# Optimization experiments

Hardware: AMD Instinct MI355X
Metric: run time of the kernel (lower is better)

The kernel has to match this reference:

```python
import jax, jax.numpy as jnp
import numpy as np

N = 50000
E = 800000
NODE_C = 96
EDGE_C = 192
C1, C2, CMU = 125, 144, 163  # round(96+96*0.3), round(96+96*0.5), round(96+96*0.7)
DIVIDER = 10.0


def setup_inputs() -> dict:
    key = jax.random.key(0)
    ks = jax.random.split(key, 32)
    def w(k, i, o):
        return jax.random.normal(k, (i, o), jnp.float32) * (1.0 / np.sqrt(i))
    inp = {
        "x": jax.random.normal(ks[0], (N, NODE_C), jnp.float32),
        "edge_index": jax.random.randint(ks[1], (2, E), 0, N, dtype=jnp.int64),
        "eps_edge": jax.random.normal(ks[2], (N, CMU), jnp.float32),
        "eps_node": jax.random.normal(ks[3], (N, NODE_C), jnp.float32),
        "w1e": w(ks[4], NODE_C, C1), "b1e": jnp.zeros((C1,), jnp.float32),
        "w2e": w(ks[5], C1, C2),     "b2e": jnp.zeros((C2,), jnp.float32),
        "wme": w(ks[6], C2, CMU),    "bme": jnp.zeros((CMU,), jnp.float32),
        "wle": w(ks[7], C2, CMU),    "ble": jnp.zeros((CMU,), jnp.float32),
        "w4e": w(ks[8], CMU, EDGE_C),"b4e": jnp.zeros((EDGE_C,), jnp.float32),
        "w1n": w(ks[9], NODE_C, NODE_C), "b1n": jnp.zeros((NODE_C,), jnp.float32),
        "wmn": w(ks[10], NODE_C, NODE_C),"bmn": jnp.zeros((NODE_C,), jnp.float32),
        "wln": w(ks[11], NODE_C, NODE_C),"bln": jnp.zeros((NODE_C,), jnp.float32),
        "w5n": w(ks[12], NODE_C, NODE_C),"b5n": jnp.zeros((NODE_C,), jnp.float32),
    }
    return inp


def reference(x, edge_index, eps_edge, eps_node,
              w1e, b1e, w2e, b2e, wme, bme, wle, ble, w4e, b4e,
              w1n, b1n, wmn, bmn, wln, bln, w5n, b5n):
    row, col = edge_index[0], edge_index[1]
    n = x.shape[0]
    # GCN symmetric normalization with self-loops (deg counts incoming edges + 1)
    deg = jax.ops.segment_sum(jnp.ones(row.shape[0], x.dtype), col, num_segments=n) + 1.0
    dinv = deg ** -0.5
    coef = dinv[row] * dinv[col]          # [E]
    self_coef = (dinv * dinv)[:, None]    # [N,1] self-loop contribution

    def conv(h, W, b):
        hw = h @ W                                            # [N, out]
        agg = jax.ops.segment_sum(hw[row] * coef[:, None], col, num_segments=n)
        return agg + hw * self_coef + b

    # edge branch
    e = jax.nn.relu(conv(x, w1e, b1e))
    e = jax.nn.relu(conv(e, w2e, b2e))
    mu_e = conv(e, wme, bme)
    ls_e = conv(e, wle, ble)
    e = mu_e + eps_edge * jnp.exp(ls_e) / DIVIDER   # training-mode reparametrize
    edges = jax.nn.sigmoid(conv(e, w4e, b4e))

    # node branch
    nn_ = jax.nn.relu(conv(x, w1n, b1n))
    mu_n = conv(nn_, wmn, bmn)
    ls_n = conv(nn_, wln, bln)
    nn_ = mu_n + eps_node * jnp.exp(ls_n) / DIVIDER
    nodes = jax.nn.relu(conv(nn_, w5n, b5n))

    return edges, nodes
```

## Files before the change

### kernel.cpp

```cpp
#include <hip/hip_runtime.h>

typedef unsigned short u16;
typedef unsigned int u32;
typedef __bf16 bf16x8 __attribute__((ext_vector_type(8)));
typedef float f32x4 __attribute__((ext_vector_type(4)));

__device__ __forceinline__ u16 f2bf(float f) {
    u32 u = __float_as_uint(f);
    u32 r = (u + 0x7fffu + ((u >> 16) & 1u)) >> 16;
    return (u16)r;
}
__device__ __forceinline__ float bf2f(u16 v) { return __uint_as_float(((u32)v) << 16); }
__device__ __forceinline__ float bf_lo(u32 v) { return __uint_as_float(v << 16); }
__device__ __forceinline__ float bf_hi(u32 v) { return __uint_as_float(v & 0xffff0000u); }
__device__ __forceinline__ u32 pack2(float lo, float hi) {
    return (u32)f2bf(lo) | (((u32)f2bf(hi)) << 16);
}


__global__ void deg_kernel(const int* __restrict__ ei, int E, int* __restrict__ cnt) {
    int i = blockIdx.x * blockDim.x + threadIdx.x;
    if (i < E) atomicAdd(&cnt[ei[E + i]], 1);
}

__global__ void dinv_kernel(const int* __restrict__ cnt, float* __restrict__ dinv, int N) {
    int i = blockIdx.x * blockDim.x + threadIdx.x;
    if (i < N) dinv[i] = 1.0f / sqrtf((float)cnt[i] + 1.0f);
}

__global__ __launch_bounds__(256) void scan1_k(const int* __restrict__ cnt,
                                               int* __restrict__ offs,
                                               int* __restrict__ bsum, int N) {
    __shared__ int lds[256];
    int t = threadIdx.x;
    int idx0 = blockIdx.x * 1024 + t * 4;
    int v[4], s = 0;
#pragma unroll
    for (int k = 0; k < 4; k++) {
        int i = idx0 + k;
        v[k] = (i < N) ? cnt[i] : 0;
        s += v[k];
    }
    lds[t] = s;
    __syncthreads();
    for (int off = 1; off < 256; off <<= 1) {
        int u = 0;
        if (t >= off) u = lds[t - off];
        __syncthreads();
        lds[t] += u;
        __syncthreads();
    }
    int run = lds[t] - s;
#pragma unroll
    for (int k = 0; k < 4; k++) {
        int i = idx0 + k;
        if (i < N) offs[i] = run;
        run += v[k];
    }
    if (t == 255) bsum[blockIdx.x] = lds[255];
}

__global__ __launch_bounds__(256) void scan2_k(int* __restrict__ bsum, int* __restrict__ boff,
                                               int nb, int* __restrict__ totp) {
    __shared__ int lds[256];
    int t = threadIdx.x;
    int s = (t < nb) ? bsum[t] : 0;
    lds[t] = s;
    __syncthreads();
    for (int off = 1; off < 256; off <<= 1) {
        int u = 0;
        if (t >= off) u = lds[t - off];
        __syncthreads();
        lds[t] += u;
        __syncthreads();
    }
    if (t < nb) boff[t] = lds[t] - s;
    if (t == 255) *totp = lds[255];
}

__global__ void scan3_k(int* __restrict__ offs, int* __restrict__ cursor,
                        const int* __restrict__ boff, int N) {
    int i = blockIdx.x * blockDim.x + threadIdx.x;
    if (i < N) {
        int v = offs[i] + boff[i >> 10];
        offs[i] = v;
        cursor[i] = v;
    }
}

__global__ void fill_kernel(const int* __restrict__ ei, int E,
                            const float* __restrict__ dinv, int* __restrict__ cursor,
                            int* __restrict__ csr_src, float* __restrict__ csr_w) {
    int i = blockIdx.x * blockDim.x + threadIdx.x;
    if (i < E) {
        int r = ei[i];
        int c = ei[E + i];
        int pos = atomicAdd(&cursor[c], 1);
        csr_src[pos] = r;
        csr_w[pos] = dinv[r];
    }
}


__global__ void cvt_f2bf_k(const float* __restrict__ src, u16* __restrict__ dst, int npairs) {
    u32* d = (u32*)dst;
    for (int i = blockIdx.x * blockDim.x + threadIdx.x; i < npairs;
         i += blockDim.x * gridDim.x) {
        float lo = src[2 * i], hi = src[2 * i + 1];
        d[i] = pack2(lo, hi);
    }
}


struct PackArgs {
    const float* W[9];
    const float* B[9];
    int Kin[9], Nout[9], KS[9], NT[9], wOff[9], bOff[9];
};

__global__ void pack_weights(PackArgs pa, u16* __restrict__ wpack, float* __restrict__ bpack) {
    int L = blockIdx.y;
    int KS = pa.KS[L], NT = pa.NT[L], Kin = pa.Kin[L], Nout = pa.Nout[L];
    int wtot = KS * NT * 512;
    int btot = NT * 16;
    const float* W = pa.W[L];
    const float* Bb = pa.B[L];
    u16* wp = wpack + pa.wOff[L];
    float* bp = bpack + pa.bOff[L];
    for (int idx = blockIdx.x * blockDim.x + threadIdx.x; idx < wtot + btot;
         idx += blockDim.x * gridDim.x) {
        if (idx < wtot) {
            int j = idx & 7;
            int lane = (idx >> 3) & 63;
            int pos = idx >> 9;
            int jt = pos % NT;
            int ks = pos / NT;
            int k = ks * 32 + ((lane >> 4) & 3) * 8 + j;
            int n = jt * 16 + (lane & 15);
            u16 v = 0;
            if (k < Kin && n < Nout) v = f2bf(W[k * Nout + n]);
            wp[idx] = v;
        } else {
            int n = idx - wtot;
            float v = 0.f;
            if (n < Nout) v = Bb[n];
            bp[n] = v;
        }
    }
}


template <int C2>
__global__ __launch_bounds__(256) void propagate_k(const u16* __restrict__ h,
                                                   u16* __restrict__ out,
                                                   const float* __restrict__ dinv,
                                                   const int* __restrict__ offs,
                                                   const int* __restrict__ csr_src,
                                                   const float* __restrict__ csr_w, int N) {
    constexpr int Cp = C2 * 2;
    const int lane = threadIdx.x & 63;
    int wid = (blockIdx.x * blockDim.x + threadIdx.x) >> 6;
    int nw = (gridDim.x * blockDim.x) >> 6;
    constexpr bool HAS1 = (C2 > 64);
    const bool a0 = lane < (C2 < 64 ? C2 : 64);
    const bool a1 = HAS1 && (lane < C2 - 64);
    const int c0 = lane, c1 = lane + 64;
    for (int n = wid; n < N; n += nw) {
        float dn = dinv[n];
        int beg = offs[n], end = offs[n + 1];
        float x0 = 0.f, y0 = 0.f, x1 = 0.f, y1 = 0.f;
        {
            const u32* hp = (const u32*)(h + (size_t)n * Cp);
            if (a0) { u32 v = hp[c0]; x0 = dn * bf_lo(v); y0 = dn * bf_hi(v); }
            if (a1) { u32 v = hp[c1]; x1 = dn * bf_lo(v); y1 = dn * bf_hi(v); }
        }
        int e = beg;
        for (; e + 1 < end; e += 2) {
            int s0 = csr_src[e], s1 = csr_src[e + 1];
            float w0 = csr_w[e], w1 = csr_w[e + 1];
            const u32* p0 = (const u32*)(h + (size_t)s0 * Cp);
            const u32* p1 = (const u32*)(h + (size_t)s1 * Cp);
            if (a0) {
                u32 u = p0[c0], v = p1[c0];
                x0 = fmaf(w0, bf_lo(u), x0); y0 = fmaf(w0, bf_hi(u), y0);
                x0 = fmaf(w1, bf_lo(v), x0); y0 = fmaf(w1, bf_hi(v), y0);
            }
            if (a1) {
                u32 u = p0[c1], v = p1[c1];
                x1 = fmaf(w0, bf_lo(u), x1); y1 = fmaf(w0, bf_hi(u), y1);
                x1 = fmaf(w1, bf_lo(v), x1); y1 = fmaf(w1, bf_hi(v), y1);
            }
        }
        if (e < end) {
            int s0 = csr_src[e];
            float w0 = csr_w[e];
            const u32* p0 = (const u32*)(h + (size_t)s0 * Cp);
            if (a0) { u32 u = p0[c0]; x0 = fmaf(w0, bf_lo(u), x0); y0 = fmaf(w0, bf_hi(u), y0); }
            if (a1) { u32 u = p0[c1]; x1 = fmaf(w0, bf_lo(u), x1); y1 = fmaf(w0, bf_hi(u), y1); }
        }
        u32* op = (u32*)(out + (size_t)n * Cp);
        if (a0) op[c0] = pack2(dn * x0, dn * y0);
        if (a1) op[c1] = pack2(dn * x1, dn * y1);
    }
}


template <int KS, int NT, int OP, int OUTF>
__global__ __launch_bounds__(256) void gemm_k(const u16* __restrict__ A,
                                              const u16* __restrict__ Bp,
                                              const float* __restrict__ bias,
                                              void* __restrict__ Cv, int M, int ldc) {
    constexpr int Kp = KS * 32;
    const int lane = threadIdx.x & 63;
    const int wave = threadIdx.x >> 6;
    int m0 = (blockIdx.x * 4 + wave) * 16;
    if (m0 >= M) return;
    int row = m0 + (lane & 15);
    if (row >= M) row = M - 1;
    const u16* aptr = A + (size_t)row * Kp + ((lane >> 4) * 8);
    const u16* bptr = Bp + lane * 8;
    f32x4 acc[NT];
#pragma unroll
    for (int j = 0; j < NT; j++) acc[j] = (f32x4){0.f, 0.f, 0.f, 0.f};
#pragma unroll
    for (int ks = 0; ks < KS; ks++) {
        bf16x8 af = *(const bf16x8*)(aptr + ks * 32);
#pragma unroll
        for (int j = 0; j < NT; j++) {
            bf16x8 bf = *(const bf16x8*)(bptr + (ks * NT + j) * 512);
            acc[j] = __builtin_amdgcn_mfma_f32_16x16x32_bf16(af, bf, acc[j], 0, 0, 0);
        }
    }
    int mrow = m0 + (lane >> 4) * 4;
#pragma unroll
    for (int j = 0; j < NT; j++) {
        int n = j * 16 + (lane & 15);
        float b = bias[n];
#pragma unroll
        for (int r = 0; r < 4; r++) {
            int m = mrow + r;
            if (m < M) {
                float v = acc[j][r] + b;
                if (OP == 1) v = fmaxf(v, 0.f);
                if (OP == 2) v = 1.f / (1.f + expf(-v));
                if (OUTF) ((float*)Cv)[(size_t)m * ldc + n] = v;
                else ((u16*)Cv)[(size_t)m * ldc + n] = f2bf(v);
            }
        }
    }
}


template <int KS, int NT1, int NT2>
__global__ __launch_bounds__(256) void gemm_dual_relu_k(const u16* __restrict__ A,
                                                        const u16* __restrict__ Bp1,
                                                        const float* __restrict__ bias1,
                                                        u16* __restrict__ C1o, int ld1,
                                                        const u16* __restrict__ Bp2,
                                                        const float* __restrict__ bias2,
                                                        u16* __restrict__ C2o, int ld2, int M) {
    constexpr int Kp = KS * 32;
    const int lane = threadIdx.x & 63;
    const int wave = threadIdx.x >> 6;
    int m0 = (blockIdx.x * 4 + wave) * 16;
    if (m0 >= M) return;
    int row = m0 + (lane & 15);
    if (row >= M) row = M - 1;
    const u16* aptr = A + (size_t)row * Kp + ((lane >> 4) * 8);
    f32x4 acc1[NT1], acc2[NT2];
#pragma unroll
    for (int j = 0; j < NT1; j++) acc1[j] = (f32x4){0.f, 0.f, 0.f, 0.f};
#pragma unroll
    for (int j = 0; j < NT2; j++) acc2[j] = (f32x4){0.f, 0.f, 0.f, 0.f};
#pragma unroll
    for (int ks = 0; ks < KS; ks++) {
        bf16x8 af = *(const bf16x8*)(aptr + ks * 32);
#pragma unroll
        for (int j = 0; j < NT1; j++) {
            bf16x8 bf = *(const bf16x8*)(Bp1 + lane * 8 + (ks * NT1 + j) * 512);
            acc1[j] = __builtin_amdgcn_mfma_f32_16x16x32_bf16(af, bf, acc1[j], 0, 0, 0);
        }
#pragma unroll
        for (int j = 0; j < NT2; j++) {
            bf16x8 bf = *(const bf16x8*)(Bp2 + lane * 8 + (ks * NT2 + j) * 512);
            acc2[j] = __builtin_amdgcn_mfma_f32_16x16x32_bf16(af, bf, acc2[j], 0, 0, 0);
        }
    }
    int mrow = m0 + (lane >> 4) * 4;
#pragma unroll
    for (int j = 0; j < NT1; j++) {
        int n = j * 16 + (lane & 15);
        float b = bias1[n];
#pragma unroll
        for (int r = 0; r < 4; r++) {
            int m = mrow + r;
            if (m < M) C1o[(size_t)m * ld1 + n] = f2bf(fmaxf(acc1[j][r] + b, 0.f));
        }
    }
#pragma unroll
    for (int j = 0; j < NT2; j++) {
        int n = j * 16 + (lane & 15);
        float b = bias2[n];
#pragma unroll
        for (int r = 0; r < 4; r++) {
            int m = mrow + r;
            if (m < M) C2o[(size_t)m * ld2 + n] = f2bf(fmaxf(acc2[j][r] + b, 0.f));
        }
    }
}


template <int KS, int NT, int CLIM>
__global__ __launch_bounds__(256) void gemm_reparam_k(const u16* __restrict__ A,
                                                      const u16* __restrict__ BpM,
                                                      const float* __restrict__ biasM,
                                                      const u16* __restrict__ BpL,
                                                      const float* __restrict__ biasL,
                                                      const float* __restrict__ eps, int epsLd,
                                                      u16* __restrict__ out, int ldc, int M) {
    constexpr int Kp = KS * 32;
    const int lane = threadIdx.x & 63;
    const int wave = threadIdx.x >> 6;
    int m0 = (blockIdx.x * 4 + wave) * 16;
    if (m0 >= M) return;
    int row = m0 + (lane & 15);
    if (row >= M) row = M - 1;
    const u16* aptr = A + (size_t)row * Kp + ((lane >> 4) * 8);
    f32x4 accM[NT], accL[NT];
#pragma unroll
    for (int j = 0; j < NT; j++) {
        accM[j] = (f32x4){0.f, 0.f, 0.f, 0.f};
        accL[j] = (f32x4){0.f, 0.f, 0.f, 0.f};
    }
#pragma unroll
    for (int ks = 0; ks < KS; ks++) {
        bf16x8 af = *(const bf16x8*)(aptr + ks * 32);
#pragma unroll
        for (int j = 0; j < NT; j++) {
            bf16x8 bm = *(const bf16x8*)(BpM + lane * 8 + (ks * NT + j) * 512);
            accM[j] = __builtin_amdgcn_mfma_f32_16x16x32_bf16(af, bm, accM[j], 0, 0, 0);
            bf16x8 bl = *(const bf16x8*)(BpL + lane * 8 + (ks * NT + j) * 512);
            accL[j] = __builtin_amdgcn_mfma_f32_16x16x32_bf16(af, bl, accL[j], 0, 0, 0);
        }
    }
    int mrow = m0 + (lane >> 4) * 4;
#pragma unroll
    for (int j = 0; j < NT; j++) {
        int n = j * 16 + (lane & 15);
        float bm = biasM[n];
        float bl = biasL[n];
#pragma unroll
        for (int r = 0; r < 4; r++) {
            int m = mrow + r;
            if (m < M) {
                float v = 0.f;
                if (n < CLIM) {
                    float e = eps[(size_t)m * epsLd + n];
                    v = (accM[j][r] + bm) + e * expf(accL[j][r] + bl) * 0.1f;
                }
                out[(size_t)m * ldc + n] = f2bf(v);
            }
        }
    }
}


extern "C" void kernel_launch(void* const* d_in, const int* in_sizes, int n_in,
                              void* d_out, int out_size, void* d_ws, size_t ws_size,
                              hipStream_t stream) {
    const float* x = (const float*)d_in[0];
    const int* ei = (const int*)d_in[1];
    const float* eps_e = (const float*)d_in[2];
    const float* eps_n = (const float*)d_in[3];
    int N = in_sizes[0] / 96;
    int E = in_sizes[1] / 2;

    char* p = (char*)d_ws;
    auto alloc = [&](size_t bytes) -> char* {
        char* r = p;
        p += (bytes + 255) & ~(size_t)255;
        return r;
    };
    int* cnt = (int*)alloc((size_t)N * 4);
    float* dinv = (float*)alloc((size_t)N * 4);
    int* offs = (int*)alloc((size_t)(N + 1) * 4);
    int* cursor = (int*)alloc((size_t)N * 4);
    int* bsum = (int*)alloc(256 * 4);
    int* boff = (int*)alloc(256 * 4);
    int* csr_src = (int*)alloc((size_t)E * 4);
    float* csr_w = (float*)alloc((size_t)E * 4);
    u16* wpack = (u16*)alloc(167936 * 2);
    float* bpack = (float*)alloc(1248 * 4);
    size_t bufBytes = (size_t)N * 192 * 2;
    u16* bufA = (u16*)alloc(bufBytes);
    u16* bufB = (u16*)alloc(bufBytes);
    u16* bufC = (u16*)alloc(bufBytes);
    u16* bufD = (u16*)alloc(bufBytes);

    hipMemsetAsync(cnt, 0, (size_t)N * 4, stream);
    int gE = (E + 255) / 256, gN = (N + 255) / 256;
    deg_kernel<<<gE, 256, 0, stream>>>(ei, E, cnt);
    dinv_kernel<<<gN, 256, 0, stream>>>(cnt, dinv, N);
    int nb = (N + 1023) / 1024;
    scan1_k<<<nb, 256, 0, stream>>>(cnt, offs, bsum, N);
    scan2_k<<<1, 256, 0, stream>>>(bsum, boff, nb, offs + N);
    scan3_k<<<gN, 256, 0, stream>>>(offs, cursor, boff, N);
    fill_kernel<<<gE, 256, 0, stream>>>(ei, E, dinv, cursor, csr_src, csr_w);

    static const int wi[9] = {4, 6, 8, 10, 12, 14, 16, 18, 20};
    static const int bi[9] = {5, 7, 9, 11, 13, 15, 17, 19, 21};
    static const int Kin[9] = {96, 125, 144, 144, 163, 96, 96, 96, 96};
    static const int Nout[9] = {125, 144, 163, 163, 192, 96, 96, 96, 96};
    static const int KSa[9] = {3, 4, 5, 5, 6, 3, 3, 3, 3};
    static const int NTa[9] = {8, 10, 12, 12, 12, 6, 6, 6, 6};
    static const int wOff[9] = {0, 12288, 32768, 63488, 94208, 131072, 140288, 149504, 158720};
    static const int bOff[9] = {0, 128, 288, 480, 672, 864, 960, 1056, 1152};
    PackArgs pa;
    for (int i = 0; i < 9; i++) {
        pa.W[i] = (const float*)d_in[wi[i]];
        pa.B[i] = (const float*)d_in[bi[i]];
        pa.Kin[i] = Kin[i]; pa.Nout[i] = Nout[i];
        pa.KS[i] = KSa[i];  pa.NT[i] = NTa[i];
        pa.wOff[i] = wOff[i]; pa.bOff[i] = bOff[i];
    }
    pack_weights<<<dim3(32, 9), 256, 0, stream>>>(pa, wpack, bpack);

    const int gp = 2048;
    const int gg = (N + 63) / 64;

    cvt_f2bf_k<<<2048, 256, 0, stream>>>(x, bufD, N * 48);
    propagate_k<48><<<gp, 256, 0, stream>>>(bufD, bufA, dinv, offs, csr_src, csr_w, N);
    gemm_dual_relu_k<3, 8, 6><<<gg, 256, 0, stream>>>(bufA, wpack + 0, bpack + 0, bufC, 128,
                                                      wpack + 131072, bpack + 864, bufB, 96, N);
    propagate_k<64><<<gp, 256, 0, stream>>>(bufC, bufA, dinv, offs, csr_src, csr_w, N);
    gemm_k<4, 10, 1, 0><<<gg, 256, 0, stream>>>(bufA, wpack + 12288, bpack + 128, bufC, N, 160);
    propagate_k<80><<<gp, 256, 0, stream>>>(bufC, bufA, dinv, offs, csr_src, csr_w, N);
    gemm_reparam_k<5, 12, 163><<<gg, 256, 0, stream>>>(bufA, wpack + 32768, bpack + 288,
                                                       wpack + 63488, bpack + 480,
                                                       eps_e, 163, bufC, 192, N);
    propagate_k<96><<<gp, 256, 0, stream>>>(bufC, bufD, dinv, offs, csr_src, csr_w, N);
    gemm_k<6, 12, 2, 1><<<gg, 256, 0, stream>>>(bufD, wpack + 94208, bpack + 672, (float*)d_out, N, 192);
    propagate_k<48><<<gp, 256, 0, stream>>>(bufB, bufA, dinv, offs, csr_src, csr_w, N);
    gemm_reparam_k<3, 6, 96><<<gg, 256, 0, stream>>>(bufA, wpack + 140288, bpack + 960,
                                                     wpack + 149504, bpack + 1056,
                                                     eps_n, 96, bufC, 96, N);
    propagate_k<48><<<gp, 256, 0, stream>>>(bufC, bufA, dinv, offs, csr_src, csr_w, N);
    gemm_k<3, 6, 1, 1><<<gg, 256, 0, stream>>>(bufA, wpack + 158720, bpack + 1152,
                                               (float*)d_out + (size_t)N * 192, N, 96);
}
```

Baseline: 792.6 us.

## Split GEMM output columns across blockIdx.y and prefetch bf16 eps before MFMA loop

Each GEMM kernel now launches a 2D grid, with blockIdx.y choosing half of the output column tiles. This doubles the number of blocks and halves the accumulators per wave, which should improve occupancy and latency hiding. The dual-relu kernel sends its two weight sets to separate y-blocks. The eps noise tensors are converted to bf16 up front, and the reparam kernels load them into registers before the matmul so the load overlaps with compute. The cost is extra conversion launches, A rows read twice, and bf16 rounding of eps.

```diff
diff --git a/kernel.cpp b/kernel.cpp
--- a/kernel.cpp
+++ b/kernel.cpp
@@ -27,6 +27,7 @@
     int i = blockIdx.x * blockDim.x + threadIdx.x;
     if (i < N) dinv[i] = 1.0f / sqrtf((float)cnt[i] + 1.0f);
 }
+
 
 __global__ __launch_bounds__(256) void scan1_k(const int* __restrict__ cnt,
                                                int* __restrict__ offs,
@@ -205,36 +206,43 @@
 }
 
 
-template <int KS, int NT, int OP, int OUTF>
+template <int KS, int NTtot, int NTH>
+__device__ __forceinline__ void gemm_body(const u16* A, const u16* Bp, int jBase,
+                                          f32x4* acc, int m0, int M, int lane) {
+    constexpr int Kp = KS * 32;
+    int row = m0 + (lane & 15);
+    if (row >= M) row = M - 1;
+    const u16* aptr = A + (size_t)row * Kp + ((lane >> 4) * 8);
+    const u16* bptr = Bp + lane * 8;
+#pragma unroll
+    for (int j = 0; j < NTH; j++) acc[j] = (f32x4){0.f, 0.f, 0.f, 0.f};
+#pragma unroll
+    for (int ks = 0; ks < KS; ks++) {
+        bf16x8 af = *(const bf16x8*)(aptr + ks * 32);
+#pragma unroll
+        for (int j = 0; j < NTH; j++) {
+            bf16x8 bf = *(const bf16x8*)(bptr + (ks * NTtot + jBase + j) * 512);
+            acc[j] = __builtin_amdgcn_mfma_f32_16x16x32_bf16(af, bf, acc[j], 0, 0, 0);
+        }
+    }
+}
+
+template <int KS, int NTtot, int NTH, int OP, int OUTF>
 __global__ __launch_bounds__(256) void gemm_k(const u16* __restrict__ A,
                                               const u16* __restrict__ Bp,
                                               const float* __restrict__ bias,
                                               void* __restrict__ Cv, int M, int ldc) {
-    constexpr int Kp = KS * 32;
     const int lane = threadIdx.x & 63;
     const int wave = threadIdx.x >> 6;
+    const int jBase = blockIdx.y * NTH;
     int m0 = (blockIdx.x * 4 + wave) * 16;
     if (m0 >= M) return;
-    int row = m0 + (lane & 15);
-    if (row >= M) row = M - 1;
-    const u16* aptr = A + (size_t)row * Kp + ((lane >> 4) * 8);
-    const u16* bptr = Bp + lane * 8;
-    f32x4 acc[NT];
-#pragma unroll
-    for (int j = 0; j < NT; j++) acc[j] = (f32x4){0.f, 0.f, 0.f, 0.f};
-#pragma unroll
-    for (int ks = 0; ks < KS; ks++) {
-        bf16x8 af = *(const bf16x8*)(aptr + ks * 32);
-#pragma unroll
-        for (int j = 0; j < NT; j++) {
-            bf16x8 bf = *(const bf16x8*)(bptr + (ks * NT + j) * 512);
-            acc[j] = __builtin_amdgcn_mfma_f32_16x16x32_bf16(af, bf, acc[j], 0, 0, 0);
-        }
-    }
+    f32x4 acc[NTH];
+    gemm_body<KS, NTtot, NTH>(A, Bp, jBase, acc, m0, M, lane);
     int mrow = m0 + (lane >> 4) * 4;
 #pragma unroll
-    for (int j = 0; j < NT; j++) {
-        int n = j * 16 + (lane & 15);
+    for (int j = 0; j < NTH; j++) {
+        int n = (jBase + j) * 16 + (lane & 15);
         float b = bias[n];
 #pragma unroll
         for (int r = 0; r < 4; r++) {
@@ -250,7 +258,6 @@
     }
 }
 
-
 template <int KS, int NT1, int NT2>
 __global__ __launch_bounds__(256) void gemm_dual_relu_k(const u16* __restrict__ A,
                                                         const u16* __restrict__ Bp1,
@@ -259,76 +266,72 @@
                                                         const u16* __restrict__ Bp2,
                                                         const float* __restrict__ bias2,
                                                         u16* __restrict__ C2o, int ld2, int M) {
-    constexpr int Kp = KS * 32;
     const int lane = threadIdx.x & 63;
     const int wave = threadIdx.x >> 6;
     int m0 = (blockIdx.x * 4 + wave) * 16;
     if (m0 >= M) return;
-    int row = m0 + (lane & 15);
-    if (row >= M) row = M - 1;
-    const u16* aptr = A + (size_t)row * Kp + ((lane >> 4) * 8);
-    f32x4 acc1[NT1], acc2[NT2];
-#pragma unroll
-    for (int j = 0; j < NT1; j++) acc1[j] = (f32x4){0.f, 0.f, 0.f, 0.f};
-#pragma unroll
-    for (int j = 0; j < NT2; j++) acc2[j] = (f32x4){0.f, 0.f, 0.f, 0.f};
-#pragma unroll
-    for (int ks = 0; ks < KS; ks++) {
-        bf16x8 af = *(const bf16x8*)(aptr + ks * 32);
+    int mrow = m0 + (lane >> 4) * 4;
+    if (blockIdx.y == 0) {
+        f32x4 acc[NT1];
+        gemm_body<KS, NT1, NT1>(A, Bp1, 0, acc, m0, M, lane);
 #pragma unroll
         for (int j = 0; j < NT1; j++) {
-            bf16x8 bf = *(const bf16x8*)(Bp1 + lane * 8 + (ks * NT1 + j) * 512);
-            acc1[j] = __builtin_amdgcn_mfma_f32_16x16x32_bf16(af, bf, acc1[j], 0, 0, 0);
-        }
+            int n = j * 16 + (lane & 15);
+            float b = bias1[n];
+#pragma unroll
+            for (int r = 0; r < 4; r++) {
+                int m = mrow + r;
+                if (m < M) C1o[(size_t)m * ld1 + n] = f2bf(fmaxf(acc[j][r] + b, 0.f));
+            }
+        }
+    } else {
+        f32x4 acc[NT2];
+        gemm_body<KS, NT2, NT2>(A, Bp2, 0, acc, m0, M, lane);
 #pragma unroll
         for (int j = 0; j < NT2; j++) {
-            bf16x8 bf = *(const bf16x8*)(Bp2 + lane * 8 + (ks * NT2 + j) * 512);
-            acc2[j] = __builtin_amdgcn_mfma_f32_16x16x32_bf16(af, bf, acc2[j], 0, 0, 0);
-        }
-    }
-    int mrow = m0 + (lane >> 4) * 4;
-#pragma unroll
-    for (int j = 0; j < NT1; j++) {
-        int n = j * 16 + (lane & 15);
-        float b = bias1[n];
-#pragma unroll
-        for (int r = 0; r < 4; r++) {
-            int m = mrow + r;
-            if (m < M) C1o[(size_t)m * ld1 + n] = f2bf(fmaxf(acc1[j][r] + b, 0.f));
-        }
-    }
-#pragma unroll
-    for (int j = 0; j < NT2; j++) {
-        int n = j * 16 + (lane & 15);
-        float b = bias2[n];
-#pragma unroll
-        for (int r = 0; r < 4; r++) {
-            int m = mrow + r;
-            if (m < M) C2o[(size_t)m * ld2 + n] = f2bf(fmaxf(acc2[j][r] + b, 0.f));
-        }
-    }
-}
-
-
-template <int KS, int NT, int CLIM>
+            int n = j * 16 + (lane & 15);
+            float b = bias2[n];
+#pragma unroll
+            for (int r = 0; r < 4; r++) {
+                int m = mrow + r;
+                if (m < M) C2o[(size_t)m * ld2 + n] = f2bf(fmaxf(acc[j][r] + b, 0.f));
+            }
+        }
+    }
+}
+
+template <int KS, int NTtot, int NTH, int CLIM>
 __global__ __launch_bounds__(256) void gemm_reparam_k(const u16* __restrict__ A,
                                                       const u16* __restrict__ BpM,
                                                       const float* __restrict__ biasM,
                                                       const u16* __restrict__ BpL,
                                                       const float* __restrict__ biasL,
-                                                      const float* __restrict__ eps, int epsLd,
+                                                      const u16* __restrict__ epsb,
                                                       u16* __restrict__ out, int ldc, int M) {
-    constexpr int Kp = KS * 32;
     const int lane = threadIdx.x & 63;
     const int wave = threadIdx.x >> 6;
+    const int jBase = blockIdx.y * NTH;
     int m0 = (blockIdx.x * 4 + wave) * 16;
     if (m0 >= M) return;
+    int mrow = m0 + (lane >> 4) * 4;
+    float epsv[NTH * 4];
+#pragma unroll
+    for (int j = 0; j < NTH; j++) {
+        int n = (jBase + j) * 16 + (lane & 15);
+#pragma unroll
+        for (int r = 0; r < 4; r++) {
+            int m = mrow + r;
+            if (m >= M) m = M - 1;
+            epsv[j * 4 + r] = (n < CLIM) ? bf2f(epsb[(size_t)m * CLIM + n]) : 0.f;
+        }
+    }
+    constexpr int Kp = KS * 32;
     int row = m0 + (lane & 15);
     if (row >= M) row = M - 1;
     const u16* aptr = A + (size_t)row * Kp + ((lane >> 4) * 8);
-    f32x4 accM[NT], accL[NT];
-#pragma unroll
-    for (int j = 0; j < NT; j++) {
+    f32x4 accM[NTH], accL[NTH];
+#pragma unroll
+    for (int j = 0; j < NTH; j++) {
         accM[j] = (f32x4){0.f, 0.f, 0.f, 0.f};
         accL[j] = (f32x4){0.f, 0.f, 0.f, 0.f};
     }
@@ -336,17 +339,16 @@
     for (int ks = 0; ks < KS; ks++) {
         bf16x8 af = *(const bf16x8*)(aptr + ks * 32);
 #pragma unroll
-        for (int j = 0; j < NT; j++) {
-            bf16x8 bm = *(const bf16x8*)(BpM + lane * 8 + (ks * NT + j) * 512);
+        for (int j = 0; j < NTH; j++) {
+            bf16x8 bm = *(const bf16x8*)(BpM + lane * 8 + (ks * NTtot + jBase + j) * 512);
             accM[j] = __builtin_amdgcn_mfma_f32_16x16x32_bf16(af, bm, accM[j], 0, 0, 0);
-            bf16x8 bl = *(const bf16x8*)(BpL + lane * 8 + (ks * NT + j) * 512);
+            bf16x8 bl = *(const bf16x8*)(BpL + lane * 8 + (ks * NTtot + jBase + j) * 512);
             accL[j] = __builtin_amdgcn_mfma_f32_16x16x32_bf16(af, bl, accL[j], 0, 0, 0);
         }
     }
-    int mrow = m0 + (lane >> 4) * 4;
-#pragma unroll
-    for (int j = 0; j < NT; j++) {
-        int n = j * 16 + (lane & 15);
+#pragma unroll
+    for (int j = 0; j < NTH; j++) {
+        int n = (jBase + j) * 16 + (lane & 15);
         float bm = biasM[n];
         float bl = biasL[n];
 #pragma unroll
@@ -354,10 +356,8 @@
             int m = mrow + r;
             if (m < M) {
                 float v = 0.f;
-                if (n < CLIM) {
-                    float e = eps[(size_t)m * epsLd + n];
-                    v = (accM[j][r] + bm) + e * expf(accL[j][r] + bl) * 0.1f;
-                }
+                if (n < CLIM)
+                    v = (accM[j][r] + bm) + epsv[j * 4 + r] * expf(accL[j][r] + bl) * 0.1f;
                 out[(size_t)m * ldc + n] = f2bf(v);
             }
         }
@@ -396,6 +396,11 @@
     u16* bufB = (u16*)alloc(bufBytes);
     u16* bufC = (u16*)alloc(bufBytes);
     u16* bufD = (u16*)alloc(bufBytes);
+    u16* epsEb = (u16*)alloc((size_t)N * 163 * 2);
+    u16* epsNb = (u16*)alloc((size_t)N * 96 * 2);
+
+    cvt_f2bf_k<<<2048, 256, 0, stream>>>(eps_e, epsEb, N * 163 / 2);
+    cvt_f2bf_k<<<2048, 256, 0, stream>>>(eps_n, epsNb, N * 48);
 
     hipMemsetAsync(cnt, 0, (size_t)N * 4, stream);
     int gE = (E + 255) / 256, gN = (N + 255) / 256;
@@ -430,21 +435,21 @@
 
     cvt_f2bf_k<<<2048, 256, 0, stream>>>(x, bufD, N * 48);
     propagate_k<48><<<gp, 256, 0, stream>>>(bufD, bufA, dinv, offs, csr_src, csr_w, N);
-    gemm_dual_relu_k<3, 8, 6><<<gg, 256, 0, stream>>>(bufA, wpack + 0, bpack + 0, bufC, 128,
-                                                      wpack + 131072, bpack + 864, bufB, 96, N);
+    gemm_dual_relu_k<3, 8, 6><<<dim3(gg, 2), 256, 0, stream>>>(
+        bufA, wpack + 0, bpack + 0, bufC, 128, wpack + 131072, bpack + 864, bufB, 96, N);
     propagate_k<64><<<gp, 256, 0, stream>>>(bufC, bufA, dinv, offs, csr_src, csr_w, N);
-    gemm_k<4, 10, 1, 0><<<gg, 256, 0, stream>>>(bufA, wpack + 12288, bpack + 128, bufC, N, 160);
+    gemm_k<4, 10, 5, 1, 0><<<dim3(gg, 2), 256, 0, stream>>>(bufA, wpack + 12288, bpack + 128,
+                                                            bufC, N, 160);
     propagate_k<80><<<gp, 256, 0, stream>>>(bufC, bufA, dinv, offs, csr_src, csr_w, N);
-    gemm_reparam_k<5, 12, 163><<<gg, 256, 0, stream>>>(bufA, wpack + 32768, bpack + 288,
-                                                       wpack + 63488, bpack + 480,
-                                                       eps_e, 163, bufC, 192, N);
+    gemm_reparam_k<5, 12, 6, 163><<<dim3(gg, 2), 256, 0, stream>>>(
+        bufA, wpack + 32768, bpack + 288, wpack + 63488, bpack + 480, epsEb, bufC, 192, N);
     propagate_k<96><<<gp, 256, 0, stream>>>(bufC, bufD, dinv, offs, csr_src, csr_w, N);
-    gemm_k<6, 12, 2, 1><<<gg, 256, 0, stream>>>(bufD, wpack + 94208, bpack + 672, (float*)d_out, N, 192);
+    gemm_k<6, 12, 6, 2, 1><<<dim3(gg, 2), 256, 0, stream>>>(bufD, wpack + 94208, bpack + 672,
+                                                            (float*)d_out, N, 192);
     propagate_k<48><<<gp, 256, 0, stream>>>(bufB, bufA, dinv, offs, csr_src, csr_w, N);
-    gemm_reparam_k<3, 6, 96><<<gg, 256, 0, stream>>>(bufA, wpack + 140288, bpack + 960,
-                                                     wpack + 149504, bpack + 1056,
-                                                     eps_n, 96, bufC, 96, N);
+    gemm_reparam_k<3, 6, 3, 96><<<dim3(gg, 2), 256, 0, stream>>>(
+        bufA, wpack + 140288, bpack + 960, wpack + 149504, bpack + 1056, epsNb, bufC, 96, N);
     propagate_k<48><<<gp, 256, 0, stream>>>(bufC, bufA, dinv, offs, csr_src, csr_w, N);
-    gemm_k<3, 6, 1, 1><<<gg, 256, 0, stream>>>(bufA, wpack + 158720, bpack + 1152,
-                                               (float*)d_out + (size_t)N * 192, N, 96);
-}
+    gemm_k<3, 6, 3, 1, 1><<<dim3(gg, 2), 256, 0, stream>>>(bufA, wpack + 158720, bpack + 1152,
+                                                           (float*)d_out + (size_t)N * 192, N, 96);
+}
```

Result: faster. 759.2 us (-4.2%).

## Fuse neighbor aggregation into MFMA GEMM kernels and pre-convert eps to bf16

Applied to the files above, without the earlier changes.

Removes the separate propagate kernels and instead gathers each node's neighbor-weighted input slice directly into the MFMA A-fragment inside each GEMM kernel, dropping one full intermediate write and read per layer and six launches. The eps noise tensors are converted to bf16 up front so the reparam epilogue reads half the bytes, at a small precision cost. Each wave now gathers 16 rows with per-lane 16-byte loads, and the edge loop differs per lane because rows have different degrees, so gather parallelism and divergence change relative to the one-wave-per-node propagate.

```diff
diff --git a/kernel.cpp b/kernel.cpp
--- a/kernel.cpp
+++ b/kernel.cpp
@@ -11,8 +11,6 @@
     return (u16)r;
 }
 __device__ __forceinline__ float bf2f(u16 v) { return __uint_as_float(((u32)v) << 16); }
-__device__ __forceinline__ float bf_lo(u32 v) { return __uint_as_float(v << 16); }
-__device__ __forceinline__ float bf_hi(u32 v) { return __uint_as_float(v & 0xffff0000u); }
 __device__ __forceinline__ u32 pack2(float lo, float hi) {
     return (u32)f2bf(lo) | (((u32)f2bf(hi)) << 16);
 }
@@ -27,6 +25,7 @@
     int i = blockIdx.x * blockDim.x + threadIdx.x;
     if (i < N) dinv[i] = 1.0f / sqrtf((float)cnt[i] + 1.0f);
 }
+
 
 __global__ __launch_bounds__(256) void scan1_k(const int* __restrict__ cnt,
                                                int* __restrict__ offs,
@@ -150,88 +149,74 @@
 }
 
 
-template <int C2>
-__global__ __launch_bounds__(256) void propagate_k(const u16* __restrict__ h,
-                                                   u16* __restrict__ out,
-                                                   const float* __restrict__ dinv,
-                                                   const int* __restrict__ offs,
-                                                   const int* __restrict__ csr_src,
-                                                   const float* __restrict__ csr_w, int N) {
-    constexpr int Cp = C2 * 2;
-    const int lane = threadIdx.x & 63;
-    int wid = (blockIdx.x * blockDim.x + threadIdx.x) >> 6;
-    int nw = (gridDim.x * blockDim.x) >> 6;
-    constexpr bool HAS1 = (C2 > 64);
-    const bool a0 = lane < (C2 < 64 ? C2 : 64);
-    const bool a1 = HAS1 && (lane < C2 - 64);
-    const int c0 = lane, c1 = lane + 64;
-    for (int n = wid; n < N; n += nw) {
-        float dn = dinv[n];
-        int beg = offs[n], end = offs[n + 1];
-        float x0 = 0.f, y0 = 0.f, x1 = 0.f, y1 = 0.f;
-        {
-            const u32* hp = (const u32*)(h + (size_t)n * Cp);
-            if (a0) { u32 v = hp[c0]; x0 = dn * bf_lo(v); y0 = dn * bf_hi(v); }
-            if (a1) { u32 v = hp[c1]; x1 = dn * bf_lo(v); y1 = dn * bf_hi(v); }
-        }
-        int e = beg;
-        for (; e + 1 < end; e += 2) {
-            int s0 = csr_src[e], s1 = csr_src[e + 1];
-            float w0 = csr_w[e], w1 = csr_w[e + 1];
-            const u32* p0 = (const u32*)(h + (size_t)s0 * Cp);
-            const u32* p1 = (const u32*)(h + (size_t)s1 * Cp);
-            if (a0) {
-                u32 u = p0[c0], v = p1[c0];
-                x0 = fmaf(w0, bf_lo(u), x0); y0 = fmaf(w0, bf_hi(u), y0);
-                x0 = fmaf(w1, bf_lo(v), x0); y0 = fmaf(w1, bf_hi(v), y0);
-            }
-            if (a1) {
-                u32 u = p0[c1], v = p1[c1];
-                x1 = fmaf(w0, bf_lo(u), x1); y1 = fmaf(w0, bf_hi(u), y1);
-                x1 = fmaf(w1, bf_lo(v), x1); y1 = fmaf(w1, bf_hi(v), y1);
-            }
-        }
-        if (e < end) {
-            int s0 = csr_src[e];
-            float w0 = csr_w[e];
-            const u32* p0 = (const u32*)(h + (size_t)s0 * Cp);
-            if (a0) { u32 u = p0[c0]; x0 = fmaf(w0, bf_lo(u), x0); y0 = fmaf(w0, bf_hi(u), y0); }
-            if (a1) { u32 u = p0[c1]; x1 = fmaf(w0, bf_lo(u), x1); y1 = fmaf(w0, bf_hi(u), y1); }
-        }
-        u32* op = (u32*)(out + (size_t)n * Cp);
-        if (a0) op[c0] = pack2(dn * x0, dn * y0);
-        if (a1) op[c1] = pack2(dn * x1, dn * y1);
-    }
-}
-
+template <int Cp>
+__device__ __forceinline__ bf16x8 gather_slice(const u16* __restrict__ h, int sliceOff,
+                                               float dn, int row, int beg, int end,
+                                               const int* __restrict__ csr_src,
+                                               const float* __restrict__ csr_w) {
+    float a[8];
+    {
+        bf16x8 sv = *(const bf16x8*)(h + (size_t)row * Cp + sliceOff);
+#pragma unroll
+        for (int j = 0; j < 8; j++) a[j] = dn * (float)sv[j];
+    }
+    int e = beg;
+    for (; e + 1 < end; e += 2) {
+        int s0 = csr_src[e], s1 = csr_src[e + 1];
+        float w0 = csr_w[e], w1 = csr_w[e + 1];
+        bf16x8 v0 = *(const bf16x8*)(h + (size_t)s0 * Cp + sliceOff);
+        bf16x8 v1 = *(const bf16x8*)(h + (size_t)s1 * Cp + sliceOff);
+#pragma unroll
+        for (int j = 0; j < 8; j++) {
+            a[j] = fmaf(w0, (float)v0[j], a[j]);
+            a[j] = fmaf(w1, (float)v1[j], a[j]);
+        }
+    }
+    if (e < end) {
+        int s0 = csr_src[e];
+        float w0 = csr_w[e];
+        bf16x8 v0 = *(const bf16x8*)(h + (size_t)s0 * Cp + sliceOff);
+#pragma unroll
+        for (int j = 0; j < 8; j++) a[j] = fmaf(w0, (float)v0[j], a[j]);
+    }
+    bf16x8 r;
+#pragma unroll
+    for (int j = 0; j < 8; j++) r[j] = (__bf16)(dn * a[j]);
+    return r;
+}
 
 template <int KS, int NT, int OP, int OUTF>
-__global__ __launch_bounds__(256) void gemm_k(const u16* __restrict__ A,
-                                              const u16* __restrict__ Bp,
-                                              const float* __restrict__ bias,
-                                              void* __restrict__ Cv, int M, int ldc) {
-    constexpr int Kp = KS * 32;
+__global__ __launch_bounds__(256) void fused_pg_k(const u16* __restrict__ h,
+                                                  const u16* __restrict__ Bp,
+                                                  const float* __restrict__ bias,
+                                                  void* __restrict__ Cv, int ldc,
+                                                  const float* __restrict__ dinv,
+                                                  const int* __restrict__ offs,
+                                                  const int* __restrict__ csr_src,
+                                                  const float* __restrict__ csr_w, int M) {
+    constexpr int Cp = KS * 32;
     const int lane = threadIdx.x & 63;
     const int wave = threadIdx.x >> 6;
     int m0 = (blockIdx.x * 4 + wave) * 16;
     if (m0 >= M) return;
     int row = m0 + (lane & 15);
     if (row >= M) row = M - 1;
-    const u16* aptr = A + (size_t)row * Kp + ((lane >> 4) * 8);
-    const u16* bptr = Bp + lane * 8;
+    const int q = lane >> 4;
+    float dn = dinv[row];
+    int beg = offs[row], end = offs[row + 1];
     f32x4 acc[NT];
 #pragma unroll
     for (int j = 0; j < NT; j++) acc[j] = (f32x4){0.f, 0.f, 0.f, 0.f};
 #pragma unroll
     for (int ks = 0; ks < KS; ks++) {
-        bf16x8 af = *(const bf16x8*)(aptr + ks * 32);
+        bf16x8 af = gather_slice<Cp>(h, ks * 32 + q * 8, dn, row, beg, end, csr_src, csr_w);
 #pragma unroll
         for (int j = 0; j < NT; j++) {
-            bf16x8 bf = *(const bf16x8*)(bptr + (ks * NT + j) * 512);
+            bf16x8 bf = *(const bf16x8*)(Bp + lane * 8 + (ks * NT + j) * 512);
             acc[j] = __builtin_amdgcn_mfma_f32_16x16x32_bf16(af, bf, acc[j], 0, 0, 0);
         }
     }
-    int mrow = m0 + (lane >> 4) * 4;
+    int mrow = m0 + q * 4;
 #pragma unroll
     for (int j = 0; j < NT; j++) {
         int n = j * 16 + (lane & 15);
@@ -250,23 +235,28 @@
     }
 }
 
-
 template <int KS, int NT1, int NT2>
-__global__ __launch_bounds__(256) void gemm_dual_relu_k(const u16* __restrict__ A,
-                                                        const u16* __restrict__ Bp1,
-                                                        const float* __restrict__ bias1,
-                                                        u16* __restrict__ C1o, int ld1,
-                                                        const u16* __restrict__ Bp2,
-                                                        const float* __restrict__ bias2,
-                                                        u16* __restrict__ C2o, int ld2, int M) {
-    constexpr int Kp = KS * 32;
+__global__ __launch_bounds__(256) void fused_pg_dual_k(const u16* __restrict__ h,
+                                                       const u16* __restrict__ Bp1,
+                                                       const float* __restrict__ bias1,
+                                                       u16* __restrict__ C1o, int ld1,
+                                                       const u16* __restrict__ Bp2,
+                                                       const float* __restrict__ bias2,
+                                                       u16* __restrict__ C2o, int ld2,
+                                                       const float* __restrict__ dinv,
+                                                       const int* __restrict__ offs,
+                                                       const int* __restrict__ csr_src,
+                                                       const float* __restrict__ csr_w, int M) {
+    constexpr int Cp = KS * 32;
     const int lane = threadIdx.x & 63;
     const int wave = threadIdx.x >> 6;
     int m0 = (blockIdx.x * 4 + wave) * 16;
     if (m0 >= M) return;
     int row = m0 + (lane & 15);
     if (row >= M) row = M - 1;
-    const u16* aptr = A + (size_t)row * Kp + ((lane >> 4) * 8);
+    const int q = lane >> 4;
+    float dn = dinv[row];
+    int beg = offs[row], end = offs[row + 1];
     f32x4 acc1[NT1], acc2[NT2];
 #pragma unroll
     for (int j = 0; j < NT1; j++) acc1[j] = (f32x4){0.f, 0.f, 0.f, 0.f};
@@ -274,7 +264,7 @@
     for (int j = 0; j < NT2; j++) acc2[j] = (f32x4){0.f, 0.f, 0.f, 0.f};
 #pragma unroll
     for (int ks = 0; ks < KS; ks++) {
-        bf16x8 af = *(const bf16x8*)(aptr + ks * 32);
+        bf16x8 af = gather_slice<Cp>(h, ks * 32 + q * 8, dn, row, beg, end, csr_src, csr_w);
 #pragma unroll
         for (int j = 0; j < NT1; j++) {
             bf16x8 bf = *(const bf16x8*)(Bp1 + lane * 8 + (ks * NT1 + j) * 512);
@@ -286,7 +276,7 @@
             acc2[j] = __builtin_amdgcn_mfma_f32_16x16x32_bf16(af, bf, acc2[j], 0, 0, 0);
         }
     }
-    int mrow = m0 + (lane >> 4) * 4;
+    int mrow = m0 + q * 4;
 #pragma unroll
     for (int j = 0; j < NT1; j++) {
         int n = j * 16 + (lane & 15);
@@ -309,23 +299,29 @@
     }
 }
 
-
 template <int KS, int NT, int CLIM>
-__global__ __launch_bounds__(256) void gemm_reparam_k(const u16* __restrict__ A,
-                                                      const u16* __restrict__ BpM,
-                                                      const float* __restrict__ biasM,
-                                                      const u16* __restrict__ BpL,
-                                                      const float* __restrict__ biasL,
-                                                      const float* __restrict__ eps, int epsLd,
-                                                      u16* __restrict__ out, int ldc, int M) {
-    constexpr int Kp = KS * 32;
+__global__ __launch_bounds__(256) void fused_pg_reparam_k(const u16* __restrict__ h,
+                                                          const u16* __restrict__ BpM,
+                                                          const float* __restrict__ biasM,
+                                                          const u16* __restrict__ BpL,
+                                                          const float* __restrict__ biasL,
+                                                          const u16* __restrict__ epsb,
+                                                          u16* __restrict__ out, int ldc,
+                                                          const float* __restrict__ dinv,
+                                                          const int* __restrict__ offs,
+                                                          const int* __restrict__ csr_src,
+                                                          const float* __restrict__ csr_w,
+                                                          int M) {
+    constexpr int Cp = KS * 32;
     const int lane = threadIdx.x & 63;
     const int wave = threadIdx.x >> 6;
     int m0 = (blockIdx.x * 4 + wave) * 16;
     if (m0 >= M) return;
     int row = m0 + (lane & 15);
     if (row >= M) row = M - 1;
-    const u16* aptr = A + (size_t)row * Kp + ((lane >> 4) * 8);
+    const int q = lane >> 4;
+    float dn = dinv[row];
+    int beg = offs[row], end = offs[row + 1];
     f32x4 accM[NT], accL[NT];
 #pragma unroll
     for (int j = 0; j < NT; j++) {
@@ -334,7 +330,7 @@
     }
 #pragma unroll
     for (int ks = 0; ks < KS; ks++) {
-        bf16x8 af = *(const bf16x8*)(aptr + ks * 32);
+        bf16x8 af = gather_slice<Cp>(h, ks * 32 + q * 8, dn, row, beg, end, csr_src, csr_w);
 #pragma unroll
         for (int j = 0; j < NT; j++) {
             bf16x8 bm = *(const bf16x8*)(BpM + lane * 8 + (ks * NT + j) * 512);
@@ -343,7 +339,7 @@
             accL[j] = __builtin_amdgcn_mfma_f32_16x16x32_bf16(af, bl, accL[j], 0, 0, 0);
         }
     }
-    int mrow = m0 + (lane >> 4) * 4;
+    int mrow = m0 + q * 4;
 #pragma unroll
     for (int j = 0; j < NT; j++) {
         int n = j * 16 + (lane & 15);
@@ -355,7 +351,7 @@
             if (m < M) {
                 float v = 0.f;
                 if (n < CLIM) {
-                    float e = eps[(size_t)m * epsLd + n];
+                    float e = bf2f(epsb[(size_t)m * CLIM + n]);
                     v = (accM[j][r] + bm) + e * expf(accL[j][r] + bl) * 0.1f;
                 }
                 out[(size_t)m * ldc + n] = f2bf(v);
@@ -396,6 +392,12 @@
     u16* bufB = (u16*)alloc(bufBytes);
     u16* bufC = (u16*)alloc(bufBytes);
     u16* bufD = (u16*)alloc(bufBytes);
+    u16* epsEb = (u16*)alloc((size_t)N * 163 * 2);
+    u16* epsNb = (u16*)alloc((size_t)N * 96 * 2);
+
+    cvt_f2bf_k<<<2048, 256, 0, stream>>>(eps_e, epsEb, N * 163 / 2);
+    cvt_f2bf_k<<<2048, 256, 0, stream>>>(eps_n, epsNb, N * 48);
+    cvt_f2bf_k<<<2048, 256, 0, stream>>>(x, bufD, N * 48);
 
     hipMemsetAsync(cnt, 0, (size_t)N * 4, stream);
     int gE = (E + 255) / 256, gN = (N + 255) / 256;
@@ -425,26 +427,22 @@
     }
     pack_weights<<<dim3(32, 9), 256, 0, stream>>>(pa, wpack, bpack);
 
-    const int gp = 2048;
     const int gg = (N + 63) / 64;
 
-    cvt_f2bf_k<<<2048, 256, 0, stream>>>(x, bufD, N * 48);
-    propagate_k<48><<<gp, 256, 0, stream>>>(bufD, bufA, dinv, offs, csr_src, csr_w, N);
-    gemm_dual_relu_k<3, 8, 6><<<gg, 256, 0, stream>>>(bufA, wpack + 0, bpack + 0, bufC, 128,
-                                                      wpack + 131072, bpack + 864, bufB, 96, N);
-    propagate_k<64><<<gp, 256, 0, stream>>>(bufC, bufA, dinv, offs, csr_src, csr_w, N);
-    gemm_k<4, 10, 1, 0><<<gg, 256, 0, stream>>>(bufA, wpack + 12288, bpack + 128, bufC, N, 160);
-    propagate_k<80><<<gp, 256, 0, stream>>>(bufC, bufA, dinv, offs, csr_src, csr_w, N);
-    gemm_reparam_k<5, 12, 163><<<gg, 256, 0, stream>>>(bufA, wpack + 32768, bpack + 288,
-                                                       wpack + 63488, bpack + 480,
-                                                       eps_e, 163, bufC, 192, N);
-    propagate_k<96><<<gp, 256, 0, stream>>>(bufC, bufD, dinv, offs, csr_src, csr_w, N);
-    gemm_k<6, 12, 2, 1><<<gg, 256, 0, stream>>>(bufD, wpack + 94208, bpack + 672, (float*)d_out, N, 192);
-    propagate_k<48><<<gp, 256, 0, stream>>>(bufB, bufA, dinv, offs, csr_src, csr_w, N);
-    gemm_reparam_k<3, 6, 96><<<gg, 256, 0, stream>>>(bufA, wpack + 140288, bpack + 960,
-                                                     wpack + 149504, bpack + 1056,
-                                                     eps_n, 96, bufC, 96, N);
-    propagate_k<48><<<gp, 256, 0, stream>>>(bufC, bufA, dinv, offs, csr_src, csr_w, N);
-    gemm_k<3, 6, 1, 1><<<gg, 256, 0, stream>>>(bufA, wpack + 158720, bpack + 1152,
-                                               (float*)d_out + (size_t)N * 192, N, 96);
-}
+    fused_pg_dual_k<3, 8, 6><<<gg, 256, 0, stream>>>(
+        bufD, wpack + 0, bpack + 0, bufC, 128, wpack + 131072, bpack + 864, bufB, 96,
+        dinv, offs, csr_src, csr_w, N);
+    fused_pg_k<4, 10, 1, 0><<<gg, 256, 0, stream>>>(
+        bufC, wpack + 12288, bpack + 128, bufA, 160, dinv, offs, csr_src, csr_w, N);
+    fused_pg_reparam_k<5, 12, 163><<<gg, 256, 0, stream>>>(
+        bufA, wpack + 32768, bpack + 288, wpack + 63488, bpack + 480, epsEb, bufC, 192,
+        dinv, offs, csr_src, csr_w, N);
+    fused_pg_k<6, 12, 2, 1><<<gg, 256, 0, stream>>>(
+        bufC, wpack + 94208, bpack + 672, (float*)d_out, 192, dinv, offs, csr_src, csr_w, N);
+    fused_pg_reparam_k<3, 6, 96><<<gg, 256, 0, stream>>>(
+        bufB, wpack + 140288, bpack + 960, wpack + 149504, bpack + 1056, epsNb, bufD, 96,
+        dinv, offs, csr_src, csr_w, N);
+    fused_pg_k<3, 6, 1, 1><<<gg, 256, 0, stream>>>(
+        bufD, wpack + 158720, bpack + 1152, (float*)d_out + (size_t)N * 192, 96,
+        dinv, offs, csr_src, csr_w, N);
+}
```

After: 820.9 us. +3.6%, slower.
